# Kernel tuning notes

Hardware: AMD Instinct MI355X
Metric: run time of the kernel (lower is better)

Reference implementation:

```python
import jax, jax.numpy as jnp
import numpy as np

N = 50000
E = 800000
IN_DIM = 128
F_NUM = 64
OUT_DIM = 16


def gcn_norm(edge_index, edge_weight, num_nodes):
    # add self loops with fill value 1.0 (improved=False), then symmetric norm
    e = edge_index.shape[1]
    w = jnp.ones((e,), jnp.float32) if edge_weight is None else edge_weight
    loop = jnp.arange(num_nodes, dtype=edge_index.dtype)
    row = jnp.concatenate([edge_index[0], loop])
    col = jnp.concatenate([edge_index[1], loop])
    w = jnp.concatenate([w, jnp.ones((num_nodes,), jnp.float32)])
    deg = jax.ops.segment_sum(w, col, num_segments=num_nodes)
    dis = jnp.where(deg > 0, jax.lax.rsqrt(jnp.where(deg > 0, deg, 1.0)), 0.0)
    norm = dis[row] * w * dis[col]
    return row, col, norm


def dgconv(x, edge_index, edge_weight, num_nodes):
    row, col, norm = gcn_norm(edge_index, edge_weight, num_nodes)
    # gather -> scale -> scatter-add
    msg = norm[:, None] * x[row]          # [E+N, F]
    return jax.ops.segment_sum(msg, col, num_segments=num_nodes)


def setup_inputs() -> dict:
    key = jax.random.key(0)
    ks = jax.random.split(key, 12)
    x = jax.random.normal(ks[0], (N, IN_DIM), jnp.float32)
    edge_index = jax.random.randint(ks[1], (2, E), 0, N, jnp.int64 if jax.config.jax_enable_x64 else jnp.int32)
    edge_in = jax.random.randint(ks[2], (2, E), 0, N, edge_index.dtype)
    edge_out = jax.random.randint(ks[3], (2, E), 0, N, edge_index.dtype)
    in_w = jax.random.uniform(ks[4], (E,), jnp.float32)
    out_w = jax.random.uniform(ks[5], (E,), jnp.float32)
    lin1_w = jax.random.normal(ks[6], (F_NUM, IN_DIM), jnp.float32) / np.sqrt(IN_DIM)
    lin2_w = jax.random.normal(ks[7], (F_NUM, 3 * F_NUM), jnp.float32) / np.sqrt(3 * F_NUM)
    bias1 = jnp.zeros((1, F_NUM), jnp.float32)
    bias2 = jnp.zeros((1, F_NUM), jnp.float32)
    conv_w = jax.random.normal(ks[8], (OUT_DIM, 3 * F_NUM), jnp.float32) / np.sqrt(3 * F_NUM)
    conv_b = jnp.zeros((OUT_DIM,), jnp.float32)
    return {"x": x, "edge_index": edge_index, "edge_in": edge_in, "edge_out": edge_out,
            "in_w": in_w, "out_w": out_w, "lin1_w": lin1_w, "lin2_w": lin2_w,
            "bias1": bias1, "bias2": bias2, "conv_w": conv_w, "conv_b": conv_b}


def reference(x, edge_index, edge_in, edge_out, in_w, out_w,
              lin1_w, lin2_w, bias1, bias2, conv_w, conv_b):
    n = x.shape[0]
    h = x @ lin1_w.T                                          # [N, F]
    h1 = dgconv(h, edge_index, None, n) + bias1
    h2 = dgconv(h, edge_in, in_w, n) + bias1
    h3 = dgconv(h, edge_out, out_w, n) + bias1
    h = jax.nn.relu(jnp.concatenate([h1, h2, h3], axis=-1))   # [N, 3F]
    h = h @ lin2_w.T                                          # [N, F]
    h1 = dgconv(h, edge_index, None, n) + bias2
    h2 = dgconv(h, edge_in, in_w, n) + bias2
    h3 = dgconv(h, edge_out, out_w, n) + bias2
    h = jax.nn.relu(jnp.concatenate([h1, h2, h3], axis=-1))   # [N, 3F]
    # Conv1d(kernel_size=1) == pointwise linear over channels
    logits = h @ conv_w.T + conv_b                            # [N, out_dim]
    return jax.nn.log_softmax(logits, axis=1)
```

## Files before the change

kernel.cpp:

```cpp
#include <hip/hip_runtime.h>
#include <hip/hip_fp16.h>
#include <math.h>

#define FDIM 64
#define CATDIM 192
#define CH 2048
#define MAXNB 1024
#define SCTILE 2048


__global__ __launch_bounds__(256) void k_chist(const int* __restrict__ ei0,
                                               const int* __restrict__ ei1,
                                               const int* __restrict__ ei2,
                                               int* __restrict__ bh,
                                               int NB, int nchunks, int E) {
    __shared__ int hist[MAXNB];
    const int c = blockIdx.x, g = blockIdx.y, tid = threadIdx.x;
    const int* dest = (g == 0 ? ei0 : g == 1 ? ei1 : ei2) + E;

    for (int i = tid; i < NB; i += 256) hist[i] = 0;
    __syncthreads();

    const int lo = c * CH, hi = min(E, lo + CH);
    for (int i = lo + tid; i < hi; i += 256) atomicAdd(&hist[dest[i] >> 6], 1);
    __syncthreads();

    for (int i = tid; i < NB; i += 256)
        bh[((size_t)g * NB + i) * nchunks + c] = hist[i];
}


__global__ __launch_bounds__(256) void k_scan_a(const int* __restrict__ bh,
                                                int* __restrict__ bsum,
                                                int L, int nblkS) {
    __shared__ int s[256];
    const int b = blockIdx.x, g = blockIdx.y, tid = threadIdx.x;
    const int* data = bh + (size_t)g * L;
    const int base = b * SCTILE + tid * 8;
    int v = 0;
#pragma unroll
    for (int j = 0; j < 8; ++j) {
        int idx = base + j;
        if (idx < L) v += data[idx];
    }
    s[tid] = v;
    __syncthreads();
    for (int d = 128; d > 0; d >>= 1) {
        if (tid < d) s[tid] += s[tid + d];
        __syncthreads();
    }
    if (tid == 0) bsum[g * nblkS + b] = s[0];
}

__global__ __launch_bounds__(256) void k_scan_b(int* __restrict__ bsum, int nblkS) {
    __shared__ int s[256];
    const int g = blockIdx.x, tid = threadIdx.x;
    int v = (tid < nblkS) ? bsum[g * nblkS + tid] : 0;
    s[tid] = v;
    __syncthreads();
    for (int d = 1; d < 256; d <<= 1) {
        int t = (tid >= d) ? s[tid - d] : 0;
        __syncthreads();
        s[tid] += t;
        __syncthreads();
    }
    if (tid < nblkS) bsum[g * nblkS + tid] = s[tid] - v;
}


__global__ __launch_bounds__(256) void k_scan_c(int* __restrict__ bh,
                                                const int* __restrict__ bsum,
                                                int* __restrict__ bbase,
                                                int L, int nblkS,
                                                int NB, int nchunks, int E) {
    __shared__ int s[256];
    const int b = blockIdx.x, g = blockIdx.y, tid = threadIdx.x;
    int* data = bh + (size_t)g * L;
    const int base = b * SCTILE + tid * 8;

    int e[8];
    int tot = 0;
#pragma unroll
    for (int j = 0; j < 8; ++j) {
        e[j] = (base + j < L) ? data[base + j] : 0;
        tot += e[j];
    }
    s[tid] = tot;
    __syncthreads();
    for (int d = 1; d < 256; d <<= 1) {
        int t = (tid >= d) ? s[tid - d] : 0;
        __syncthreads();
        s[tid] += t;
        __syncthreads();
    }
    int run = bsum[g * nblkS + b] + s[tid] - tot;
#pragma unroll
    for (int j = 0; j < 8; ++j) {
        int idx = base + j;
        if (idx < L) {
            int v = e[j];
            data[idx] = run;
            if (idx % nchunks == 0) bbase[g * (NB + 1) + idx / nchunks] = run;
            run += v;
        }
    }
    if (b == 0 && tid == 0) bbase[g * (NB + 1) + NB] = E;
}


__global__ __launch_bounds__(256) void k_cfill(const int* __restrict__ ei0,
                                               const int* __restrict__ ei1,
                                               const int* __restrict__ ei2,
                                               const float* __restrict__ w1,
                                               const float* __restrict__ w2,
                                               const int* __restrict__ bhs,
                                               int2* __restrict__ barr,
                                               int NB, int nchunks, int E) {
    __shared__ int cur[MAXNB];
    const int c = blockIdx.x, g = blockIdx.y, tid = threadIdx.x;
    const int* e = (g == 0 ? ei0 : g == 1 ? ei1 : ei2);
    const float* w = (g == 1 ? w1 : w2);
    const int* srcp = e;
    const int* dest = e + E;
    int2* bout = barr + (size_t)g * E;

    for (int i = tid; i < NB; i += 256)
        cur[i] = bhs[((size_t)g * NB + i) * nchunks + c];
    __syncthreads();

    const int lo = c * CH, hi = min(E, lo + CH);
    for (int i = lo + tid; i < hi; i += 256) {
        int d = dest[i];
        int slot = atomicAdd(&cur[d >> 6], 1);
        float wv = (g == 0) ? 0.f : w[i];
        bout[slot] = make_int2(srcp[i] | ((d & 63) << 16), __float_as_int(wv));
    }
}


__global__ __launch_bounds__(256) void k_deg(const int2* __restrict__ barr,
                                             const int* __restrict__ bbase,
                                             int* __restrict__ rowptr,
                                             float* __restrict__ dis,
                                             int N, int E, int NB) {
    __shared__ int hist[64];
    __shared__ float wsum[64];
    __shared__ int sc[64];

    const int b = blockIdx.x, g = blockIdx.y, tid = threadIdx.x;
    const int2* bin = barr + (size_t)g * E;
    const int beg = bbase[g * (NB + 1) + b];
    const int end = bbase[g * (NB + 1) + b + 1];

    if (tid < 64) { hist[tid] = 0; wsum[tid] = 1.0f; }
    __syncthreads();

    for (int t = beg + tid; t < end; t += 256) {
        int2 p = bin[t];
        int dl = (p.x >> 16) & 63;
        atomicAdd(&hist[dl], 1);
        if (g) atomicAdd(&wsum[dl], __int_as_float(p.y));
    }
    __syncthreads();

    if (tid < 64) sc[tid] = hist[tid];
    __syncthreads();
    for (int d = 1; d < 64; d <<= 1) {
        int t = 0;
        if (tid < 64 && tid >= d) t = sc[tid - d];
        __syncthreads();
        if (tid < 64) sc[tid] += t;
        __syncthreads();
    }
    if (tid < 64) {
        int node = b * 64 + tid;
        if (node < N) {
            rowptr[g * (N + 1) + node] = beg + (sc[tid] - hist[tid]);
            float s = g ? wsum[tid] : (1.0f + (float)hist[tid]);
            dis[g * N + node] = rsqrtf(s);
        }
    }
    if (b == NB - 1 && tid == 0) rowptr[g * (N + 1) + N] = end;
}


__global__ __launch_bounds__(256) void k_place(const int2* __restrict__ barr,
                                               const int* __restrict__ bbase,
                                               const int* __restrict__ rowptr,
                                               const float* __restrict__ dis,
                                               unsigned* __restrict__ csr,
                                               int N, int E, int NB) {
    __shared__ int cur[64];
    const int b = blockIdx.x, g = blockIdx.y, tid = threadIdx.x;
    const int2* bin = barr + (size_t)g * E;
    const int beg = bbase[g * (NB + 1) + b];
    const int end = bbase[g * (NB + 1) + b + 1];

    if (tid < 64) {
        int node = b * 64 + tid;
        cur[tid] = (node < N) ? rowptr[g * (N + 1) + node] - beg : 0;
    }
    __syncthreads();

    for (int t = beg + tid; t < end; t += 256) {
        int2 p = bin[t];
        int dl = (p.x >> 16) & 63;
        int pos = atomicAdd(&cur[dl], 1);
        int src = p.x & 0xFFFF;
        float wv = g ? __int_as_float(p.y) : 1.0f;
        float v = wv * dis[g * N + src];
        unsigned short wb = __half_as_ushort(__float2half(v));
        csr[(size_t)g * E + beg + pos] = (unsigned)src | ((unsigned)wb << 16);
    }
}


template <typename T> __device__ inline float4 load4f(const T* p);
template <> __device__ inline float4 load4f<float>(const float* p) {
    return *reinterpret_cast<const float4*>(p);
}
template <> __device__ inline float4 load4f<__half>(const __half* p) {
    __half2 a = *reinterpret_cast<const __half2*>(p);
    __half2 b = *reinterpret_cast<const __half2*>(p + 2);
    float2 fa = __half22float2(a), fb = __half22float2(b);
    return make_float4(fa.x, fa.y, fb.x, fb.y);
}

template <int K, int KCH, typename TA>
__global__ __launch_bounds__(256) void k_gemm(const TA* __restrict__ A,
                                              const float* __restrict__ W,
                                              __half* __restrict__ out, int n) {
    __shared__ float wt[KCH * 65];
    __shared__ float xs[64 * 36];

    const int tid = threadIdx.x;
    const int n0 = blockIdx.x * 64;

    const int f = tid & 63;
    const int q = tid >> 6;
    float acc[16];
#pragma unroll
    for (int j = 0; j < 16; ++j) acc[j] = 0.f;

    for (int kc = 0; kc < K; kc += 32) {
        __syncthreads();
        if ((kc % KCH) == 0) {
            for (int idx = tid; idx < FDIM * KCH; idx += 256) {
                int fr = idx / KCH;
                int kr = idx - fr * KCH;
                wt[kr * 65 + fr] = W[fr * K + kc + kr];
            }
        }
#pragma unroll
        for (int u = tid; u < 512; u += 256) {
            int node = u >> 3;
            int k4 = u & 7;
            int gn = n0 + node;
            float4 a = make_float4(0.f, 0.f, 0.f, 0.f);
            if (gn < n) a = load4f(&A[(size_t)gn * K + kc + k4 * 4]);
            *reinterpret_cast<float4*>(&xs[node * 36 + k4 * 4]) = a;
        }
        __syncthreads();

        const int kb = kc % KCH;
#pragma unroll
        for (int kk = 0; kk < 32; kk += 4) {
            float w0 = wt[(kb + kk + 0) * 65 + f];
            float w1 = wt[(kb + kk + 1) * 65 + f];
            float w2 = wt[(kb + kk + 2) * 65 + f];
            float w3 = wt[(kb + kk + 3) * 65 + f];
#pragma unroll
            for (int jj = 0; jj < 16; ++jj) {
                int j = jj * 4 + q;
                float4 av = *reinterpret_cast<const float4*>(&xs[j * 36 + kk]);
                acc[jj] = fmaf(av.x, w0, fmaf(av.y, w1, fmaf(av.z, w2, fmaf(av.w, w3, acc[jj]))));
            }
        }
    }

#pragma unroll
    for (int jj = 0; jj < 16; ++jj) {
        int node = n0 + jj * 4 + q;
        if (node < n) out[(size_t)node * FDIM + f] = __float2half(acc[jj]);
    }
}


__global__ __launch_bounds__(256) void k_gather(const __half* __restrict__ h,
                                                const float* __restrict__ dis,
                                                const int* __restrict__ rowptr,
                                                const unsigned* __restrict__ csr,
                                                const float* __restrict__ bias,
                                                __half* __restrict__ cat,
                                                int N, int E) {
    int i = blockIdx.x * 4 + (threadIdx.x >> 6);
    if (i >= N) return;
    const int lane = threadIdx.x & 63;

    const float hv = __half2float(h[(size_t)i * FDIM + lane]);
    const float b = bias[lane];

#pragma unroll
    for (int g = 0; g < 3; ++g) {
        const int* rp = rowptr + g * (N + 1);
        const unsigned* cg = csr + (size_t)g * E;
        const int beg = __builtin_amdgcn_readfirstlane(rp[i]);
        const int end = __builtin_amdgcn_readfirstlane(rp[i + 1]);
        float dg = dis[g * N + i];

        float acc0 = 0.f, acc1 = 0.f, acc2 = 0.f, acc3 = 0.f;
        float acc4 = 0.f, acc5 = 0.f, acc6 = 0.f, acc7 = 0.f;
        int j = beg;
        for (; j + 8 <= end; j += 8) {
            unsigned u0 = cg[j + 0];
            unsigned u1 = cg[j + 1];
            unsigned u2 = cg[j + 2];
            unsigned u3 = cg[j + 3];
            unsigned u4 = cg[j + 4];
            unsigned u5 = cg[j + 5];
            unsigned u6 = cg[j + 6];
            unsigned u7 = cg[j + 7];
            float a0 = __half2float(h[(size_t)(u0 & 0xFFFFu) * FDIM + lane]);
            float a1 = __half2float(h[(size_t)(u1 & 0xFFFFu) * FDIM + lane]);
            float a2 = __half2float(h[(size_t)(u2 & 0xFFFFu) * FDIM + lane]);
            float a3 = __half2float(h[(size_t)(u3 & 0xFFFFu) * FDIM + lane]);
            float a4 = __half2float(h[(size_t)(u4 & 0xFFFFu) * FDIM + lane]);
            float a5 = __half2float(h[(size_t)(u5 & 0xFFFFu) * FDIM + lane]);
            float a6 = __half2float(h[(size_t)(u6 & 0xFFFFu) * FDIM + lane]);
            float a7 = __half2float(h[(size_t)(u7 & 0xFFFFu) * FDIM + lane]);
            acc0 = fmaf(__half2float(__ushort_as_half((unsigned short)(u0 >> 16))), a0, acc0);
            acc1 = fmaf(__half2float(__ushort_as_half((unsigned short)(u1 >> 16))), a1, acc1);
            acc2 = fmaf(__half2float(__ushort_as_half((unsigned short)(u2 >> 16))), a2, acc2);
            acc3 = fmaf(__half2float(__ushort_as_half((unsigned short)(u3 >> 16))), a3, acc3);
            acc4 = fmaf(__half2float(__ushort_as_half((unsigned short)(u4 >> 16))), a4, acc4);
            acc5 = fmaf(__half2float(__ushort_as_half((unsigned short)(u5 >> 16))), a5, acc5);
            acc6 = fmaf(__half2float(__ushort_as_half((unsigned short)(u6 >> 16))), a6, acc6);
            acc7 = fmaf(__half2float(__ushort_as_half((unsigned short)(u7 >> 16))), a7, acc7);
        }
        if (j + 4 <= end) {
            unsigned u0 = cg[j + 0];
            unsigned u1 = cg[j + 1];
            unsigned u2 = cg[j + 2];
            unsigned u3 = cg[j + 3];
            float a0 = __half2float(h[(size_t)(u0 & 0xFFFFu) * FDIM + lane]);
            float a1 = __half2float(h[(size_t)(u1 & 0xFFFFu) * FDIM + lane]);
            float a2 = __half2float(h[(size_t)(u2 & 0xFFFFu) * FDIM + lane]);
            float a3 = __half2float(h[(size_t)(u3 & 0xFFFFu) * FDIM + lane]);
            acc0 = fmaf(__half2float(__ushort_as_half((unsigned short)(u0 >> 16))), a0, acc0);
            acc1 = fmaf(__half2float(__ushort_as_half((unsigned short)(u1 >> 16))), a1, acc1);
            acc2 = fmaf(__half2float(__ushort_as_half((unsigned short)(u2 >> 16))), a2, acc2);
            acc3 = fmaf(__half2float(__ushort_as_half((unsigned short)(u3 >> 16))), a3, acc3);
            j += 4;
        }
        for (; j < end; ++j) {
            unsigned u0 = cg[j];
            float a0 = __half2float(h[(size_t)(u0 & 0xFFFFu) * FDIM + lane]);
            acc0 = fmaf(__half2float(__ushort_as_half((unsigned short)(u0 >> 16))), a0, acc0);
        }
        float outv = dg * (((acc0 + acc1) + (acc2 + acc3)) + ((acc4 + acc5) + (acc6 + acc7)))
                   + dg * dg * hv + b;
        cat[(size_t)i * CATDIM + g * FDIM + lane] = __float2half(outv > 0.f ? outv : 0.f);
    }
}


__global__ __launch_bounds__(256) void k_final(const __half* __restrict__ cat,
                                               const float* __restrict__ convw,
                                               const float* __restrict__ convb,
                                               float* __restrict__ out, int n) {
    __shared__ float wl[16 * 196];
    __shared__ float bl[16];
    const int tid = threadIdx.x;
    for (int t = tid; t < 16 * 192; t += 256) {
        int o = t / 192;
        int k = t - o * 192;
        wl[o * 196 + k] = convw[t];
    }
    if (tid < 16) bl[tid] = convb[tid];
    __syncthreads();

    const int o = tid & 15;
    const int node = blockIdx.x * 16 + (tid >> 4);
    const int nc = node < n ? node : n - 1;

    const float4* xr4 = reinterpret_cast<const float4*>(cat + (size_t)nc * CATDIM);
    const float* wr = &wl[o * 196];
    float acc = bl[o];
#pragma unroll
    for (int k8 = 0; k8 < CATDIM / 8; ++k8) {
        float4 raw = xr4[k8];
        const __half2* hp = reinterpret_cast<const __half2*>(&raw);
        float2 f0 = __half22float2(hp[0]);
        float2 f1 = __half22float2(hp[1]);
        float2 f2 = __half22float2(hp[2]);
        float2 f3 = __half22float2(hp[3]);
        const float* w8 = wr + k8 * 8;
        acc += f0.x * w8[0] + f0.y * w8[1] + f1.x * w8[2] + f1.y * w8[3] +
               f2.x * w8[4] + f2.y * w8[5] + f3.x * w8[6] + f3.y * w8[7];
    }

    float m = acc;
    m = fmaxf(m, __shfl_xor(m, 1));
    m = fmaxf(m, __shfl_xor(m, 2));
    m = fmaxf(m, __shfl_xor(m, 4));
    m = fmaxf(m, __shfl_xor(m, 8));
    float s = __expf(acc - m);
    s += __shfl_xor(s, 1);
    s += __shfl_xor(s, 2);
    s += __shfl_xor(s, 4);
    s += __shfl_xor(s, 8);
    if (node < n) out[(size_t)node * 16 + o] = acc - m - logf(s);
}


extern "C" void kernel_launch(void* const* d_in, const int* in_sizes, int n_in,
                              void* d_out, int out_size, void* d_ws, size_t ws_size,
                              hipStream_t stream) {
    const float* x      = (const float*)d_in[0];
    const int*   ei     = (const int*)d_in[1];
    const int*   e_in   = (const int*)d_in[2];
    const int*   e_out  = (const int*)d_in[3];
    const float* in_w   = (const float*)d_in[4];
    const float* out_w  = (const float*)d_in[5];
    const float* lin1_w = (const float*)d_in[6];
    const float* lin2_w = (const float*)d_in[7];
    const float* bias1  = (const float*)d_in[8];
    const float* bias2  = (const float*)d_in[9];
    const float* conv_w = (const float*)d_in[10];
    const float* conv_b = (const float*)d_in[11];
    float* out = (float*)d_out;

    const int N = in_sizes[0] / 128;
    const int E = in_sizes[1] / 2;
    const int NB = (N + 63) >> 6;
    const int nchunks = (E + CH - 1) / CH;
    const int L = NB * nchunks;
    const int nblkS = (L + SCTILE - 1) / SCTILE;

    float* ws = (float*)d_ws;
    size_t o = 0;
    float* dis    = ws + o;            o += (size_t)3 * N;
    int*   rowptr = (int*)(ws + o);    o += ((size_t)3 * (N + 1) + 1) & ~1ull;
    int*   bbase  = (int*)(ws + o);    o += ((size_t)3 * (NB + 1) + 1) & ~1ull;
    int*   bsum   = (int*)(ws + o);    o += ((size_t)3 * nblkS + 1) & ~1ull;
    int*   bh     = (int*)(ws + o);    o += ((size_t)3 * L + 3) & ~3ull;
    __half* h     = (__half*)(ws + o); o += (size_t)N * (FDIM / 2);
    o = (o + 3) & ~3ull;
    unsigned* csr = (unsigned*)(ws + o); o += (size_t)3 * E;
    o = (o + 3) & ~3ull;
    __half* cat   = (__half*)(ws + o); o += (size_t)N * (CATDIM / 2);
    int2*  barr   = (int2*)cat;

    const int B = 256;

    hipLaunchKernelGGL(k_chist, dim3(nchunks, 3), dim3(B), 0, stream, ei, e_in, e_out, bh, NB, nchunks, E);
    hipLaunchKernelGGL(k_scan_a, dim3(nblkS, 3), dim3(B), 0, stream, bh, bsum, L, nblkS);
    hipLaunchKernelGGL(k_scan_b, dim3(3), dim3(B), 0, stream, bsum, nblkS);
    hipLaunchKernelGGL(k_scan_c, dim3(nblkS, 3), dim3(B), 0, stream, bh, bsum, bbase, L, nblkS, NB, nchunks, E);
    hipLaunchKernelGGL(k_cfill, dim3(nchunks, 3), dim3(B), 0, stream,
                       ei, e_in, e_out, in_w, out_w, bh, barr, NB, nchunks, E);
    hipLaunchKernelGGL(k_deg, dim3(NB, 3), dim3(B), 0, stream, barr, bbase, rowptr, dis, N, E, NB);
    hipLaunchKernelGGL(k_place, dim3(NB, 3), dim3(B), 0, stream, barr, bbase, rowptr, dis, csr, N, E, NB);

    hipLaunchKernelGGL((k_gemm<128, 64, float>), dim3((N + 63) / 64), dim3(B), 0, stream, x, lin1_w, h, N);
    hipLaunchKernelGGL(k_gather, dim3((N + 3) / 4), dim3(B), 0, stream,
                       h, dis, rowptr, csr, bias1, cat, N, E);

    hipLaunchKernelGGL((k_gemm<192, 96, __half>), dim3((N + 63) / 64), dim3(B), 0, stream, cat, lin2_w, h, N);
    hipLaunchKernelGGL(k_gather, dim3((N + 3) / 4), dim3(B), 0, stream,
                       h, dis, rowptr, csr, bias2, cat, N, E);

    hipLaunchKernelGGL(k_final, dim3((N + 15) / 16), dim3(B), 0, stream, cat, conv_w, conv_b, out, N);
}
```

Before: 393.3 us.

## Split features into two halves and gather each half with edge-parallel lanes

The GEMM now writes h in a feature-partitioned layout, two planes of N×32 halves, instead of N×64. The gather kernel becomes a template that runs once per feature half. In each wavefront, four lane groups each take a different edge and load half2 pairs, then combine their partial sums with cross-lane shuffles before writing into the unchanged concatenated layout. The goal is a per-pass gather working set of about half the size, which should fit cache better, with fewer load instructions per edge. In exchange it adds a second launch per layer, reads the CSR arrays twice, and adds shuffle reductions and lane-select logic.

```diff
diff --git a/kernel.cpp b/kernel.cpp
--- a/kernel.cpp
+++ b/kernel.cpp
@@ -278,27 +278,36 @@
         }
     }
 
+    const int p = f >> 5, fl = f & 31;
 #pragma unroll
     for (int jj = 0; jj < 16; ++jj) {
         int node = n0 + jj * 4 + q;
-        if (node < n) out[(size_t)node * FDIM + f] = __float2half(acc[jj]);
-    }
-}
-
-
-__global__ __launch_bounds__(256) void k_gather(const __half* __restrict__ h,
+        if (node < n)
+            out[((size_t)p * n + node) * 32 + fl] = __float2half(acc[jj]);
+    }
+}
+
+
+template <int P>
+__global__ __launch_bounds__(256) void k_gather(const __half* __restrict__ hh,
                                                 const float* __restrict__ dis,
                                                 const int* __restrict__ rowptr,
                                                 const unsigned* __restrict__ csr,
                                                 const float* __restrict__ bias,
                                                 __half* __restrict__ cat,
                                                 int N, int E) {
-    int i = blockIdx.x * 4 + (threadIdx.x >> 6);
+    const int i = blockIdx.x * 4 + (threadIdx.x >> 6);
     if (i >= N) return;
     const int lane = threadIdx.x & 63;
-
-    const float hv = __half2float(h[(size_t)i * FDIM + lane]);
-    const float b = bias[lane];
+    const int fpair = lane & 15;
+    const bool e0 = (lane & 16) != 0;
+    const bool e1 = (lane & 32) != 0;
+
+    const __half2* h2 = reinterpret_cast<const __half2*>(hh) + (size_t)P * N * 16;
+    const float2 hv = __half22float2(h2[(size_t)i * 16 + fpair]);
+    const float b0 = bias[P * 32 + fpair * 2];
+    const float b1 = bias[P * 32 + fpair * 2 + 1];
+    __half2* c2 = reinterpret_cast<__half2*>(cat);
 
 #pragma unroll
     for (int g = 0; g < 3; ++g) {
@@ -306,60 +315,50 @@
         const unsigned* cg = csr + (size_t)g * E;
         const int beg = __builtin_amdgcn_readfirstlane(rp[i]);
         const int end = __builtin_amdgcn_readfirstlane(rp[i + 1]);
-        float dg = dis[g * N + i];
-
-        float acc0 = 0.f, acc1 = 0.f, acc2 = 0.f, acc3 = 0.f;
-        float acc4 = 0.f, acc5 = 0.f, acc6 = 0.f, acc7 = 0.f;
+        const float dg = dis[g * N + i];
+
+        float ax0 = 0.f, ay0 = 0.f, ax1 = 0.f, ay1 = 0.f;
         int j = beg;
         for (; j + 8 <= end; j += 8) {
-            unsigned u0 = cg[j + 0];
-            unsigned u1 = cg[j + 1];
-            unsigned u2 = cg[j + 2];
-            unsigned u3 = cg[j + 3];
-            unsigned u4 = cg[j + 4];
-            unsigned u5 = cg[j + 5];
-            unsigned u6 = cg[j + 6];
-            unsigned u7 = cg[j + 7];
-            float a0 = __half2float(h[(size_t)(u0 & 0xFFFFu) * FDIM + lane]);
-            float a1 = __half2float(h[(size_t)(u1 & 0xFFFFu) * FDIM + lane]);
-            float a2 = __half2float(h[(size_t)(u2 & 0xFFFFu) * FDIM + lane]);
-            float a3 = __half2float(h[(size_t)(u3 & 0xFFFFu) * FDIM + lane]);
-            float a4 = __half2float(h[(size_t)(u4 & 0xFFFFu) * FDIM + lane]);
-            float a5 = __half2float(h[(size_t)(u5 & 0xFFFFu) * FDIM + lane]);
-            float a6 = __half2float(h[(size_t)(u6 & 0xFFFFu) * FDIM + lane]);
-            float a7 = __half2float(h[(size_t)(u7 & 0xFFFFu) * FDIM + lane]);
-            acc0 = fmaf(__half2float(__ushort_as_half((unsigned short)(u0 >> 16))), a0, acc0);
-            acc1 = fmaf(__half2float(__ushort_as_half((unsigned short)(u1 >> 16))), a1, acc1);
-            acc2 = fmaf(__half2float(__ushort_as_half((unsigned short)(u2 >> 16))), a2, acc2);
-            acc3 = fmaf(__half2float(__ushort_as_half((unsigned short)(u3 >> 16))), a3, acc3);
-            acc4 = fmaf(__half2float(__ushort_as_half((unsigned short)(u4 >> 16))), a4, acc4);
-            acc5 = fmaf(__half2float(__ushort_as_half((unsigned short)(u5 >> 16))), a5, acc5);
-            acc6 = fmaf(__half2float(__ushort_as_half((unsigned short)(u6 >> 16))), a6, acc6);
-            acc7 = fmaf(__half2float(__ushort_as_half((unsigned short)(u7 >> 16))), a7, acc7);
-        }
-        if (j + 4 <= end) {
-            unsigned u0 = cg[j + 0];
-            unsigned u1 = cg[j + 1];
-            unsigned u2 = cg[j + 2];
-            unsigned u3 = cg[j + 3];
-            float a0 = __half2float(h[(size_t)(u0 & 0xFFFFu) * FDIM + lane]);
-            float a1 = __half2float(h[(size_t)(u1 & 0xFFFFu) * FDIM + lane]);
-            float a2 = __half2float(h[(size_t)(u2 & 0xFFFFu) * FDIM + lane]);
-            float a3 = __half2float(h[(size_t)(u3 & 0xFFFFu) * FDIM + lane]);
-            acc0 = fmaf(__half2float(__ushort_as_half((unsigned short)(u0 >> 16))), a0, acc0);
-            acc1 = fmaf(__half2float(__ushort_as_half((unsigned short)(u1 >> 16))), a1, acc1);
-            acc2 = fmaf(__half2float(__ushort_as_half((unsigned short)(u2 >> 16))), a2, acc2);
-            acc3 = fmaf(__half2float(__ushort_as_half((unsigned short)(u3 >> 16))), a3, acc3);
-            j += 4;
-        }
-        for (; j < end; ++j) {
+            unsigned u0 = cg[j + 0], u1 = cg[j + 1], u2 = cg[j + 2], u3 = cg[j + 3];
+            unsigned u4 = cg[j + 4], u5 = cg[j + 5], u6 = cg[j + 6], u7 = cg[j + 7];
+            unsigned ua = e1 ? (e0 ? u3 : u2) : (e0 ? u1 : u0);
+            unsigned ub = e1 ? (e0 ? u7 : u6) : (e0 ? u5 : u4);
+            float2 A = __half22float2(h2[(size_t)(ua & 0xFFFFu) * 16 + fpair]);
+            float2 Bv = __half22float2(h2[(size_t)(ub & 0xFFFFu) * 16 + fpair]);
+            float wa = __half2float(__ushort_as_half((unsigned short)(ua >> 16)));
+            float wb = __half2float(__ushort_as_half((unsigned short)(ub >> 16)));
+            ax0 = fmaf(wa, A.x, ax0);
+            ay0 = fmaf(wa, A.y, ay0);
+            ax1 = fmaf(wb, Bv.x, ax1);
+            ay1 = fmaf(wb, Bv.y, ay1);
+        }
+        for (; j < end; j += 4) {
+            const int jm = end - 1;
             unsigned u0 = cg[j];
-            float a0 = __half2float(h[(size_t)(u0 & 0xFFFFu) * FDIM + lane]);
-            acc0 = fmaf(__half2float(__ushort_as_half((unsigned short)(u0 >> 16))), a0, acc0);
-        }
-        float outv = dg * (((acc0 + acc1) + (acc2 + acc3)) + ((acc4 + acc5) + (acc6 + acc7)))
-                   + dg * dg * hv + b;
-        cat[(size_t)i * CATDIM + g * FDIM + lane] = __float2half(outv > 0.f ? outv : 0.f);
+            unsigned u1 = (j + 1 <= jm) ? cg[j + 1] : 0u;
+            unsigned u2 = (j + 2 <= jm) ? cg[j + 2] : 0u;
+            unsigned u3 = (j + 3 <= jm) ? cg[j + 3] : 0u;
+            unsigned ua = e1 ? (e0 ? u3 : u2) : (e0 ? u1 : u0);
+            float2 A = __half22float2(h2[(size_t)(ua & 0xFFFFu) * 16 + fpair]);
+            float wa = __half2float(__ushort_as_half((unsigned short)(ua >> 16)));
+            ax0 = fmaf(wa, A.x, ax0);
+            ay0 = fmaf(wa, A.y, ay0);
+        }
+
+        float sx = ax0 + ax1;
+        float sy = ay0 + ay1;
+        sx += __shfl_xor(sx, 16);
+        sy += __shfl_xor(sy, 16);
+        sx += __shfl_xor(sx, 32);
+        sy += __shfl_xor(sy, 32);
+        if (lane < 16) {
+            float r0 = fmaf(dg, sx, dg * dg * hv.x) + b0;
+            float r1 = fmaf(dg, sy, dg * dg * hv.y) + b1;
+            r0 = r0 > 0.f ? r0 : 0.f;
+            r1 = r1 > 0.f ? r1 : 0.f;
+            c2[(size_t)i * 96 + g * 32 + P * 16 + fpair] = __floats2half2_rn(r0, r1);
+        }
     }
 }
 
@@ -463,12 +462,16 @@
     hipLaunchKernelGGL(k_place, dim3(NB, 3), dim3(B), 0, stream, barr, bbase, rowptr, dis, csr, N, E, NB);
 
     hipLaunchKernelGGL((k_gemm<128, 64, float>), dim3((N + 63) / 64), dim3(B), 0, stream, x, lin1_w, h, N);
-    hipLaunchKernelGGL(k_gather, dim3((N + 3) / 4), dim3(B), 0, stream,
+    hipLaunchKernelGGL((k_gather<0>), dim3((N + 3) / 4), dim3(B), 0, stream,
                        h, dis, rowptr, csr, bias1, cat, N, E);
+    hipLaunchKernelGGL((k_gather<1>), dim3((N + 3) / 4), dim3(B), 0, stream,
+                       h, dis, rowptr, csr, bias1, cat, N, E);
 
     hipLaunchKernelGGL((k_gemm<192, 96, __half>), dim3((N + 63) / 64), dim3(B), 0, stream, cat, lin2_w, h, N);
-    hipLaunchKernelGGL(k_gather, dim3((N + 3) / 4), dim3(B), 0, stream,
+    hipLaunchKernelGGL((k_gather<0>), dim3((N + 3) / 4), dim3(B), 0, stream,
                        h, dis, rowptr, csr, bias2, cat, N, E);
+    hipLaunchKernelGGL((k_gather<1>), dim3((N + 3) / 4), dim3(B), 0, stream,
+                       h, dis, rowptr, csr, bias2, cat, N, E);
 
     hipLaunchKernelGGL(k_final, dim3((N + 15) / 16), dim3(B), 0, stream, cat, conv_w, conv_b, out, N);
 }
```

Result: slower. 460.1 us (+17.0%).
